# Kernel tuning notes

Hardware: AMD Instinct MI355X
Metric: run time of the kernel (lower is better)

The kernel has to match this reference:

```python
import jax, jax.numpy as jnp
import numpy as np

MIN_NORM = 1e-15
EPS = 1e-5
C_CURV = 1.0  # args.c

def _norm(x):
    return jnp.clip(jnp.linalg.norm(x, axis=-1, keepdims=True), MIN_NORM)

def artanh(x):
    x = jnp.clip(x, -1.0 + EPS, 1.0 - EPS)
    return 0.5 * (jnp.log1p(x) - jnp.log1p(-x))

def proj(x, c):
    # clip points to stay strictly inside the Poincare ball
    norm = _norm(x)
    maxnorm = (1.0 - EPS) / jnp.sqrt(c)
    return jnp.where(norm > maxnorm, x / norm * maxnorm, x)

def expmap0(u, c):
    sqrt_c = jnp.sqrt(c)
    u_norm = _norm(u)
    return jnp.tanh(sqrt_c * u_norm) * u / (sqrt_c * u_norm)

def logmap0(p, c):
    sqrt_c = jnp.sqrt(c)
    p_norm = _norm(p)
    return artanh(sqrt_c * p_norm) * p / (sqrt_c * p_norm)

def mobius_add(x, y, c):
    x2 = jnp.sum(x * x, axis=-1, keepdims=True)
    y2 = jnp.sum(y * y, axis=-1, keepdims=True)
    xy = jnp.sum(x * y, axis=-1, keepdims=True)
    num = (1.0 + 2.0 * c * xy + c * y2) * x + (1.0 - c * x2) * y
    denom = 1.0 + 2.0 * c * xy + c * c * x2 * y2
    return num / jnp.clip(denom, MIN_NORM)

def mobius_matvec(W, x, c):
    sqrt_c = jnp.sqrt(c)
    x_norm = _norm(x)
    mx = x @ W.T
    mx_norm = _norm(mx)
    return jnp.tanh(mx_norm / x_norm * artanh(sqrt_c * x_norm)) * mx / (mx_norm * sqrt_c)

def poincare_dist(x, y, c):
    sqrt_c = jnp.sqrt(c)
    d = _norm(mobius_add(-x, y, c))[..., 0]
    return 2.0 / sqrt_c * artanh(sqrt_c * d)

def hgnn_layer(h, adj, W, b, c):
    # HypLinear: mobius matvec + hyperbolic bias
    mv = proj(mobius_matvec(W, h, c), c)
    hyp_b = proj(expmap0(b, c), c)
    h = proj(mobius_add(mv, hyp_b, c), c)
    # HypAgg: aggregate in tangent space at origin
    h = proj(expmap0(adj @ logmap0(h, c), c), c)
    # HypAct: relu in tangent space
    return proj(expmap0(jax.nn.relu(logmap0(h, c)), c), c)

def setup_inputs() -> dict:
    key = jax.random.key(0)
    ks = jax.random.split(key, 10)
    N, D, C, NC, NODE_C, L = 8192, 128, 64, 7, 7, 4
    x = jax.random.normal(ks[0], (N, D), jnp.float32)
    adj = jax.random.uniform(ks[1], (N, N), jnp.float32) / N  # row-stochastic-ish dense adjacency
    graph_indicator = jax.random.randint(ks[2], (N,), 0, 1)
    W_conv = jax.random.normal(ks[3], (L, D, D), jnp.float32) / np.sqrt(D)
    b_conv = jax.random.normal(ks[4], (L, D), jnp.float32) * 0.01
    centroids = jax.random.normal(ks[5], (C, D), jnp.float32) * 0.1
    W_mlp = jax.random.normal(ks[6], (NC, C), jnp.float32) * 0.1
    b_mlp = jnp.zeros((NC,), jnp.float32)
    W_mlp1 = jax.random.normal(ks[7], (NODE_C, D), jnp.float32) * 0.1
    b_mlp1 = jnp.zeros((NODE_C,), jnp.float32)
    return {"x": x, "adj": adj, "graph_indicator": graph_indicator,
            "W_conv": W_conv, "b_conv": b_conv, "centroids": centroids,
            "W_mlp": W_mlp, "b_mlp": b_mlp, "W_mlp1": W_mlp1, "b_mlp1": b_mlp1}

def reference(x, adj, graph_indicator, W_conv, b_conv, centroids, W_mlp, b_mlp, W_mlp1, b_mlp1):
    c = C_CURV
    # proj_tan0 is identity for PoincareBall
    h = proj(expmap0(x, c), c)
    # 2 residual blocks, each with 2 HGNN layers; shortcut is identity (in_dim == out_dim)
    for blk in range(2):
        res = h
        for j in range(2):
            idx = blk * 2 + j
            h = hgnn_layer(h, adj, W_conv[idx], b_conv[idx], c)
        h = h + res  # Euclidean residual, as in the source
    # CentroidDistance: pairwise hyperbolic distance [N, C]
    node_centroid_dist = poincare_dist(h[:, None, :], centroids[None, :, :], c)
    readout = jnp.mean(node_centroid_dist, axis=0, keepdims=True)  # [1, C]
    h_r = logmap0(readout, c)  # proj_tan0(logmap0(.)) -> identity proj_tan0
    logits = jax.nn.softmax(h_r @ W_mlp.T + b_mlp, axis=0)[None]        # [1,1,NC]
    h1 = logmap0(h, c)
    logits_node = jax.nn.softmax(h1 @ W_mlp1.T + b_mlp1, axis=0)[None]  # [1,N,node_classes]
    return (logits, logits_node, h_r)
```

## Files before the change

### kernel.cpp

```cpp
#include <hip/hip_runtime.h>

#define MIN_NORM 1e-15f
#define EPSV 1e-5f
#define MAXN (1.0f - EPSV)
#define NN 8192
#define DD 128

typedef unsigned short u16;
typedef __bf16 bf16x8 __attribute__((ext_vector_type(8)));
typedef float f32x4 __attribute__((ext_vector_type(4)));

__device__ __forceinline__ float wave_sum(float v) {
#pragma unroll
  for (int off = 32; off > 0; off >>= 1) v += __shfl_xor(v, off, 64);
  return v;
}

__device__ __forceinline__ float artanh_f(float x) {
  x = fminf(fmaxf(x, -1.0f + EPSV), 1.0f - EPSV);
  return 0.5f * (log1pf(x) - log1pf(-x));
}

__device__ __forceinline__ u16 f2bf(float f) {
  unsigned u = __float_as_uint(f);
  unsigned r = (u + 0x7fffu + ((u >> 16) & 1u)) >> 16;
  return (u16)r;
}
__device__ __forceinline__ float bf2f(u16 b) { return __uint_as_float(((unsigned)b) << 16); }

__device__ __forceinline__ void gload16(const u16* g, u16* l) {
  __builtin_amdgcn_global_load_lds((const __attribute__((address_space(1))) void*)(g),
                                   (__attribute__((address_space(3))) void*)(l), 16, 0, 0);
}

__global__ __launch_bounds__(256) void gemm_bt(const u16* __restrict__ A,
                                               const u16* __restrict__ Bt,
                                               float* __restrict__ Cp,
                                               int M, int K, int KC) {
  __shared__ __align__(16) u16 Ash[2 * 64 * 64];
  __shared__ __align__(16) u16 Bsh[2 * 128 * 64];

  const int tid = threadIdx.x;
  const int lane = tid & 63;
  const int w = tid >> 6;
  const int wm = w >> 1, wn = w & 1;
  const int lrow = lane & 15;
  const int lq = lane >> 4;
  const int m0 = blockIdx.x * 64;
  const int kk0 = blockIdx.y * KC;

  const int srow = lane >> 3;
  const int spc = lane & 7;

  const u16* Ap = A + (size_t)m0 * K;

  f32x4 acc[2][4];
#pragma unroll
  for (int a = 0; a < 2; a++)
#pragma unroll
    for (int b = 0; b < 4; b++)
#pragma unroll
      for (int r = 0; r < 4; r++) acc[a][b][r] = 0.0f;

#define STAGE(bf, kk)                                                          \
  do {                                                                         \
    _Pragma("unroll") for (int ii = 0; ii < 2; ii++) {                         \
      int rw = ((ii * 4 + w) << 3) + srow;                                     \
      gload16(Ap + (size_t)rw * K + (kk) + ((spc ^ (rw & 7)) << 3),            \
              &Ash[(bf) * 4096 + ((ii * 4 + w) << 9)]);                        \
    }                                                                          \
    _Pragma("unroll") for (int ii = 0; ii < 4; ii++) {                         \
      int rw = ((ii * 4 + w) << 3) + srow;                                     \
      gload16(Bt + (size_t)rw * K + (kk) + ((spc ^ (rw & 7)) << 3),            \
              &Bsh[(bf) * 8192 + ((ii * 4 + w) << 9)]);                        \
    }                                                                          \
  } while (0)

  const int nt = KC >> 6;
  STAGE(0, kk0);

  for (int t = 0; t < nt; t++) {
    const int cur = t & 1;
    __syncthreads();
    if (t + 1 < nt) STAGE(cur ^ 1, kk0 + (t + 1) * 64);

    const int abase = cur * 4096, bbase = cur * 8192;
#pragma unroll
    for (int ks = 0; ks < 2; ks++) {
      const int lc = ks * 4 + lq;
      bf16x8 af[2], bfr[4];
#pragma unroll
      for (int ti = 0; ti < 2; ti++) {
        int r = wm * 32 + ti * 16 + lrow;
        af[ti] = *(const bf16x8*)&Ash[abase + r * 64 + ((lc ^ (r & 7)) << 3)];
      }
#pragma unroll
      for (int tj = 0; tj < 4; tj++) {
        int n = wn * 64 + tj * 16 + lrow;
        bfr[tj] = *(const bf16x8*)&Bsh[bbase + n * 64 + ((lc ^ (n & 7)) << 3)];
      }
#pragma unroll
      for (int ti = 0; ti < 2; ti++)
#pragma unroll
        for (int tj = 0; tj < 4; tj++)
          acc[ti][tj] = __builtin_amdgcn_mfma_f32_16x16x32_bf16(af[ti], bfr[tj], acc[ti][tj], 0, 0, 0);
    }
  }
#undef STAGE

  float* C = Cp + (size_t)blockIdx.y * M * 128;
#pragma unroll
  for (int ti = 0; ti < 2; ti++)
#pragma unroll
    for (int tj = 0; tj < 4; tj++)
#pragma unroll
      for (int r = 0; r < 4; r++) {
        int row = m0 + wm * 32 + ti * 16 + lq * 4 + r;
        int col = wn * 64 + tj * 16 + lrow;
        C[(size_t)row * 128 + col] = acc[ti][tj][r];
      }
}

__global__ __launch_bounds__(256) void cvt_adj(const float* __restrict__ src,
                                               u16* __restrict__ dst) {
  const size_t stride = (size_t)gridDim.x * 256 * 8;
  for (size_t base = ((size_t)blockIdx.x * 256 + threadIdx.x) * 8;
       base < (size_t)NN * NN; base += stride) {
    float4 a = *(const float4*)(src + base);
    float4 b = *(const float4*)(src + base + 4);
    ushort4 d0, d1;
    d0.x = f2bf(a.x); d0.y = f2bf(a.y); d0.z = f2bf(a.z); d0.w = f2bf(a.w);
    d1.x = f2bf(b.x); d1.y = f2bf(b.y); d1.z = f2bf(b.z); d1.w = f2bf(b.w);
    *(ushort4*)(dst + base) = d0;
    *(ushort4*)(dst + base + 4) = d1;
  }
}

__global__ void build_wt(const float* __restrict__ W, u16* __restrict__ Wt2) {
  int idx = blockIdx.x * 256 + threadIdx.x;
  if (idx >= 4 * 128 * 128) return;
  int layer = idx >> 14;
  int n = (idx >> 7) & 127;
  int k = idx & 127;
  float e = W[idx];
  u16 hi = f2bf(e);
  u16 lo = f2bf(e - bf2f(hi));
  u16* base = Wt2 + (size_t)layer * 128 * 384 + (size_t)n * 384;
  base[k] = hi;
  base[128 + k] = hi;
  base[256 + k] = lo;
}

__device__ __forceinline__ void write_split(u16* hs, int i, int lane, float v0, float v1) {
  u16* row = hs + (size_t)i * 384;
  u16 h0 = f2bf(v0), h1 = f2bf(v1);
  u16 l0 = f2bf(v0 - bf2f(h0)), l1 = f2bf(v1 - bf2f(h1));
  row[lane] = h0;         row[lane + 64] = h1;
  row[128 + lane] = l0;   row[128 + 64 + lane] = l1;
  row[256 + lane] = h0;   row[256 + 64 + lane] = h1;
}

__global__ __launch_bounds__(64) void rowwise_init(const float* __restrict__ x,
                                                   float* __restrict__ h,
                                                   float* __restrict__ res,
                                                   u16* __restrict__ hsplit) {
  int i = blockIdx.x, lane = threadIdx.x;
  const float* xr = x + (size_t)i * DD;
  float a0 = xr[lane], a1 = xr[lane + 64];
  float n = fmaxf(sqrtf(wave_sum(a0 * a0 + a1 * a1)), MIN_NORM);
  float g = tanhf(n) / n;
  float y0 = g * a0, y1 = g * a1;
  float pn = fmaxf(sqrtf(wave_sum(y0 * y0 + y1 * y1)), MIN_NORM);
  float s = pn > MAXN ? MAXN / pn : 1.0f;
  y0 *= s; y1 *= s;
  size_t base = (size_t)i * DD;
  h[base + lane] = y0;   h[base + lane + 64] = y1;
  res[base + lane] = y0; res[base + lane + 64] = y1;
  write_split(hsplit, i, lane, y0, y1);
}

__global__ __launch_bounds__(64) void rowwise_mid(const float* __restrict__ h,
                                                  const float* __restrict__ P,
                                                  const float* __restrict__ bvec,
                                                  u16* __restrict__ uT) {
  int i = blockIdx.x, lane = threadIdx.x;
  size_t base = (size_t)i * DD;
  const float* hr = h + base;
  float h0 = hr[lane], h1 = hr[lane + 64];
  float m0 = 0.f, m1 = 0.f;
#pragma unroll
  for (int sk = 0; sk < 3; sk++) {
    const float* p = P + (size_t)sk * NN * DD + base;
    m0 += p[lane];
    m1 += p[lane + 64];
  }
  float xn = fmaxf(sqrtf(wave_sum(h0 * h0 + h1 * h1)), MIN_NORM);
  float mn = fmaxf(sqrtf(wave_sum(m0 * m0 + m1 * m1)), MIN_NORM);
  float t = tanhf(mn / xn * artanh_f(xn));
  float v0 = t * m0 / mn, v1 = t * m1 / mn;
  float pn = fmaxf(sqrtf(wave_sum(v0 * v0 + v1 * v1)), MIN_NORM);
  float sc = pn > MAXN ? MAXN / pn : 1.0f;
  v0 *= sc; v1 *= sc;
  float b0 = bvec[lane], b1 = bvec[lane + 64];
  float bn = fmaxf(sqrtf(wave_sum(b0 * b0 + b1 * b1)), MIN_NORM);
  float gb = tanhf(bn) / bn;
  float e0 = gb * b0, e1 = gb * b1;
  float en = fmaxf(sqrtf(wave_sum(e0 * e0 + e1 * e1)), MIN_NORM);
  float sb = en > MAXN ? MAXN / en : 1.0f;
  e0 *= sb; e1 *= sb;
  float x2 = wave_sum(v0 * v0 + v1 * v1);
  float y2 = wave_sum(e0 * e0 + e1 * e1);
  float xy = wave_sum(v0 * e0 + v1 * e1);
  float ca = 1.0f + 2.0f * xy + y2;
  float cb = 1.0f - x2;
  float den = fmaxf(1.0f + 2.0f * xy + x2 * y2, MIN_NORM);
  float t0 = (ca * v0 + cb * e0) / den, t1 = (ca * v1 + cb * e1) / den;
  float tn = fmaxf(sqrtf(wave_sum(t0 * t0 + t1 * t1)), MIN_NORM);
  float st = tn > MAXN ? MAXN / tn : 1.0f;
  t0 *= st; t1 *= st;
  float pn2 = fmaxf(sqrtf(wave_sum(t0 * t0 + t1 * t1)), MIN_NORM);
  float gl = artanh_f(pn2) / pn2;
  uT[(size_t)lane * NN + i] = f2bf(gl * t0);
  uT[(size_t)(lane + 64) * NN + i] = f2bf(gl * t1);
}

__global__ __launch_bounds__(64) void rowwise_post(const float* __restrict__ P,
                                                   float* __restrict__ h,
                                                   float* __restrict__ res,
                                                   u16* __restrict__ hsplit,
                                                   int addres) {
  int i = blockIdx.x, lane = threadIdx.x;
  size_t base = (size_t)i * DD;
  float m0 = 0.f, m1 = 0.f;
#pragma unroll
  for (int sk = 0; sk < 8; sk++) {
    const float* p = P + (size_t)sk * NN * DD + base;
    m0 += p[lane];
    m1 += p[lane + 64];
  }
  float n = fmaxf(sqrtf(wave_sum(m0 * m0 + m1 * m1)), MIN_NORM);
  float g = tanhf(n) / n;
  float y0 = g * m0, y1 = g * m1;
  float pn = fmaxf(sqrtf(wave_sum(y0 * y0 + y1 * y1)), MIN_NORM);
  float s = pn > MAXN ? MAXN / pn : 1.0f;
  y0 *= s; y1 *= s;
  float hn = fmaxf(sqrtf(wave_sum(y0 * y0 + y1 * y1)), MIN_NORM);
  float gl = artanh_f(hn) / hn;
  float u0 = fmaxf(gl * y0, 0.0f), u1 = fmaxf(gl * y1, 0.0f);
  float un = fmaxf(sqrtf(wave_sum(u0 * u0 + u1 * u1)), MIN_NORM);
  float ge = tanhf(un) / un;
  float z0 = ge * u0, z1 = ge * u1;
  float zn = fmaxf(sqrtf(wave_sum(z0 * z0 + z1 * z1)), MIN_NORM);
  float sz = zn > MAXN ? MAXN / zn : 1.0f;
  z0 *= sz; z1 *= sz;
  if (addres) {
    z0 += res[base + lane];
    z1 += res[base + lane + 64];
    res[base + lane] = z0;
    res[base + lane + 64] = z1;
  }
  h[base + lane] = z0;
  h[base + lane + 64] = z1;
  write_split(hsplit, i, lane, z0, z1);
}

__global__ __launch_bounds__(256) void centroid_k(const float* __restrict__ h,
                                                  const float* __restrict__ cen,
                                                  float* __restrict__ rs) {
  __shared__ float cs[64 * 129];
  __shared__ float hs[32 * 128];
  __shared__ float y2s[64];
  int tid = threadIdx.x;
  int i0 = blockIdx.x * 32;
  for (int idx = tid; idx < 64 * 128; idx += 256) {
    int r = idx >> 7, c = idx & 127;
    cs[r * 129 + c] = cen[idx];
  }
  for (int idx = tid; idx < 32 * 128; idx += 256) hs[idx] = h[(size_t)i0 * 128 + idx];
  __syncthreads();
  if (tid < 64) {
    float s = 0.f;
    for (int k = 0; k < 128; k++) { float v = cs[tid * 129 + k]; s = fmaf(v, v, s); }
    y2s[tid] = s;
  }
  __syncthreads();
  int w = tid >> 6, lane = tid & 63;
  float dsum = 0.f;
  for (int rr = 0; rr < 8; rr++) {
    int r = w * 8 + rr;
    float dot = 0.f, x2 = 0.f;
    for (int k = 0; k < 128; k++) {
      float hk = hs[r * 128 + k];
      dot = fmaf(hk, cs[lane * 129 + k], dot);
      x2 = fmaf(hk, hk, x2);
    }
    float y2 = y2s[lane];
    float al = 1.0f - 2.0f * dot + y2;
    float be = 1.0f - x2;
    float num2 = al * al * x2 + be * be * y2 - 2.0f * al * be * dot;
    float den = fmaxf(1.0f - 2.0f * dot + x2 * y2, MIN_NORM);
    float d = fmaxf(sqrtf(fmaxf(num2, 0.0f)) / den, MIN_NORM);
    dsum += 2.0f * artanh_f(d);
  }
  atomicAdd(&rs[lane], dsum);
}

__global__ __launch_bounds__(64) void finalize_k(const float* __restrict__ rs,
                                                 float* __restrict__ out) {
  int lane = threadIdx.x;
  float r = rs[lane] * (1.0f / 8192.0f);
  float n = fmaxf(sqrtf(wave_sum(r * r)), MIN_NORM);
  float a = artanh_f(n);
  out[7 + NN * 7 + lane] = a * r / n;
  if (lane < 7) out[lane] = 1.0f;
}

__global__ __launch_bounds__(64) void scores_k(const float* __restrict__ h,
                                               const float* __restrict__ Wm,
                                               const float* __restrict__ bm,
                                               float* __restrict__ sc) {
  int i = blockIdx.x, lane = threadIdx.x;
  const float* hr = h + (size_t)i * DD;
  float h0 = hr[lane], h1 = hr[lane + 64];
  float pn = fmaxf(sqrtf(wave_sum(h0 * h0 + h1 * h1)), MIN_NORM);
  float gl = artanh_f(pn) / pn;
  float u0 = gl * h0, u1 = gl * h1;
  float p[7];
#pragma unroll
  for (int j = 0; j < 7; j++)
    p[j] = wave_sum(u0 * Wm[j * 128 + lane] + u1 * Wm[j * 128 + lane + 64]);
  float v = p[0];
#pragma unroll
  for (int j = 1; j < 7; j++)
    if (lane == j) v = p[j];
  if (lane < 7) sc[(size_t)i * 7 + lane] = v + bm[lane];
}

__global__ __launch_bounds__(256) void softmax_col(const float* __restrict__ sc,
                                                   float* __restrict__ out) {
  __shared__ float buf[256][8];
  int tid = threadIdx.x;
  float mx[7];
#pragma unroll
  for (int j = 0; j < 7; j++) mx[j] = -1e30f;
  for (int i = tid; i < NN; i += 256)
#pragma unroll
    for (int j = 0; j < 7; j++) mx[j] = fmaxf(mx[j], sc[i * 7 + j]);
#pragma unroll
  for (int j = 0; j < 7; j++) buf[tid][j] = mx[j];
  __syncthreads();
  for (int off = 128; off > 0; off >>= 1) {
    if (tid < off)
#pragma unroll
      for (int j = 0; j < 7; j++) buf[tid][j] = fmaxf(buf[tid][j], buf[tid + off][j]);
    __syncthreads();
  }
  float cm[7];
#pragma unroll
  for (int j = 0; j < 7; j++) cm[j] = buf[0][j];
  __syncthreads();
  float sm[7];
#pragma unroll
  for (int j = 0; j < 7; j++) sm[j] = 0.f;
  for (int i = tid; i < NN; i += 256)
#pragma unroll
    for (int j = 0; j < 7; j++) sm[j] += expf(sc[i * 7 + j] - cm[j]);
#pragma unroll
  for (int j = 0; j < 7; j++) buf[tid][j] = sm[j];
  __syncthreads();
  for (int off = 128; off > 0; off >>= 1) {
    if (tid < off)
#pragma unroll
      for (int j = 0; j < 7; j++) buf[tid][j] += buf[tid + off][j];
    __syncthreads();
  }
  float csum[7];
#pragma unroll
  for (int j = 0; j < 7; j++) csum[j] = buf[0][j];
  __syncthreads();
  for (int idx = tid; idx < NN * 7; idx += 256) {
    int i = idx / 7, j = idx - i * 7;
    out[idx] = expf(sc[i * 7 + j] - cm[j]) / csum[j];
  }
}

extern "C" void kernel_launch(void* const* d_in, const int* in_sizes, int n_in,
                              void* d_out, int out_size, void* d_ws, size_t ws_size,
                              hipStream_t stream) {
  const float* x = (const float*)d_in[0];
  const float* adj = (const float*)d_in[1];
  const float* W_conv = (const float*)d_in[3];
  const float* b_conv = (const float*)d_in[4];
  const float* centroids = (const float*)d_in[5];
  const float* W_mlp1 = (const float*)d_in[8];
  const float* b_mlp1 = (const float*)d_in[9];
  float* out = (float*)d_out;

  char* ws = (char*)d_ws;
  size_t off = 0;
  auto alloc = [&](size_t bytes) {
    void* p = ws + off;
    off = (off + bytes + 255) & ~(size_t)255;
    return p;
  };
  float* h = (float*)alloc((size_t)NN * DD * 4);
  float* res = (float*)alloc((size_t)NN * DD * 4);
  u16* hsplit = (u16*)alloc((size_t)NN * 384 * 2);
  u16* uT = (u16*)alloc((size_t)DD * NN * 2);
  u16* Wt2 = (u16*)alloc((size_t)4 * 128 * 384 * 2);
  float* P = (float*)alloc((size_t)8 * NN * DD * 4);
  u16* adjbf = (u16*)alloc((size_t)NN * NN * 2);
  float* scores = (float*)alloc((size_t)NN * 7 * 4);
  float* rs = (float*)alloc(64 * 4);
  (void)ws_size; (void)in_sizes; (void)n_in; (void)out_size;

  hipMemsetAsync(rs, 0, 64 * 4, stream);
  build_wt<<<(4 * 128 * 128 + 255) / 256, 256, 0, stream>>>(W_conv, Wt2);
  rowwise_init<<<NN, 64, 0, stream>>>(x, h, res, hsplit);
  cvt_adj<<<2048, 256, 0, stream>>>(adj, adjbf);
  for (int layer = 0; layer < 4; layer++) {
    gemm_bt<<<dim3(NN / 64, 3), 256, 0, stream>>>(
        hsplit, Wt2 + (size_t)layer * 128 * 384, P, NN, 384, 128);
    rowwise_mid<<<NN, 64, 0, stream>>>(h, P, b_conv + layer * DD, uT);
    gemm_bt<<<dim3(NN / 64, 8), 256, 0, stream>>>(
        adjbf, uT, P, NN, NN, NN / 8);
    rowwise_post<<<NN, 64, 0, stream>>>(P, h, res, hsplit, (layer & 1));
  }
  centroid_k<<<256, 256, 0, stream>>>(h, centroids, rs);
  finalize_k<<<1, 64, 0, stream>>>(rs, out);
  scores_k<<<NN, 64, 0, stream>>>(h, W_mlp1, b_mlp1, scores);
  softmax_col<<<1, 256, 0, stream>>>(scores, out + 7);
}
```

Measured before the change: 817.3 us.

## Pre-tile and pre-swizzle adjacency and uT into contiguous 64x64 GEMM tiles

The bf16 conversion of adj now writes the matrix as contiguous, pre-swizzled 64x64 tiles, and rowwise_mid writes uT in a matching tiled layout. The adjacency GEMM gets a templated TILED path, so each wave's global-to-LDS loads read one contiguous 4KB/8KB block instead of strided rows. This targets DRAM/TLB locality and address arithmetic in the dominant adj@u GEMM. The cost is scattered 2-byte writes in rowwise_mid and a more complex conversion kernel.

```diff
diff --git a/kernel.cpp b/kernel.cpp
--- a/kernel.cpp
+++ b/kernel.cpp
@@ -33,6 +33,7 @@
                                    (__attribute__((address_space(3))) void*)(l), 16, 0, 0);
 }
 
+template <bool TILED>
 __global__ __launch_bounds__(256) void gemm_bt(const u16* __restrict__ A,
                                                const u16* __restrict__ Bt,
                                                float* __restrict__ Cp,
@@ -48,11 +49,13 @@
   const int lq = lane >> 4;
   const int m0 = blockIdx.x * 64;
   const int kk0 = blockIdx.y * KC;
+  const int kt0 = kk0 >> 6;
+  const int bxK = blockIdx.x * (K >> 6);
 
   const int srow = lane >> 3;
   const int spc = lane & 7;
 
-  const u16* Ap = A + (size_t)m0 * K;
+  const u16* Ap = A + (TILED ? 0 : (size_t)m0 * K);
 
   f32x4 acc[2][4];
 #pragma unroll
@@ -62,27 +65,36 @@
 #pragma unroll
       for (int r = 0; r < 4; r++) acc[a][b][r] = 0.0f;
 
-#define STAGE(bf, kk)                                                          \
+#define STAGE(bf, tkt, kk)                                                     \
   do {                                                                         \
-    _Pragma("unroll") for (int ii = 0; ii < 2; ii++) {                         \
-      int rw = ((ii * 4 + w) << 3) + srow;                                     \
-      gload16(Ap + (size_t)rw * K + (kk) + ((spc ^ (rw & 7)) << 3),            \
-              &Ash[(bf) * 4096 + ((ii * 4 + w) << 9)]);                        \
-    }                                                                          \
-    _Pragma("unroll") for (int ii = 0; ii < 4; ii++) {                         \
-      int rw = ((ii * 4 + w) << 3) + srow;                                     \
-      gload16(Bt + (size_t)rw * K + (kk) + ((spc ^ (rw & 7)) << 3),            \
-              &Bsh[(bf) * 8192 + ((ii * 4 + w) << 9)]);                        \
+    if constexpr (TILED) {                                                     \
+      const u16* at = A + (((size_t)(bxK + (tkt))) << 12) + (lane << 3);       \
+      _Pragma("unroll") for (int ii = 0; ii < 2; ii++)                         \
+        gload16(at + ((ii * 4 + w) << 9), &Ash[(bf) * 4096 + ((ii * 4 + w) << 9)]); \
+      const u16* bt2 = Bt + (((size_t)(tkt)) << 13) + (lane << 3);             \
+      _Pragma("unroll") for (int ii = 0; ii < 4; ii++)                         \
+        gload16(bt2 + ((ii * 4 + w) << 9), &Bsh[(bf) * 8192 + ((ii * 4 + w) << 9)]); \
+    } else {                                                                   \
+      _Pragma("unroll") for (int ii = 0; ii < 2; ii++) {                       \
+        int rw = ((ii * 4 + w) << 3) + srow;                                   \
+        gload16(Ap + (size_t)rw * K + (kk) + ((spc ^ (rw & 7)) << 3),          \
+                &Ash[(bf) * 4096 + ((ii * 4 + w) << 9)]);                      \
+      }                                                                        \
+      _Pragma("unroll") for (int ii = 0; ii < 4; ii++) {                       \
+        int rw = ((ii * 4 + w) << 3) + srow;                                   \
+        gload16(Bt + (size_t)rw * K + (kk) + ((spc ^ (rw & 7)) << 3),          \
+                &Bsh[(bf) * 8192 + ((ii * 4 + w) << 9)]);                      \
+      }                                                                        \
     }                                                                          \
   } while (0)
 
   const int nt = KC >> 6;
-  STAGE(0, kk0);
+  STAGE(0, kt0, kk0);
 
   for (int t = 0; t < nt; t++) {
     const int cur = t & 1;
     __syncthreads();
-    if (t + 1 < nt) STAGE(cur ^ 1, kk0 + (t + 1) * 64);
+    if (t + 1 < nt) STAGE(cur ^ 1, kt0 + t + 1, kk0 + (t + 1) * 64);
 
     const int abase = cur * 4096, bbase = cur * 8192;
 #pragma unroll
@@ -121,18 +133,27 @@
       }
 }
 
-__global__ __launch_bounds__(256) void cvt_adj(const float* __restrict__ src,
-                                               u16* __restrict__ dst) {
-  const size_t stride = (size_t)gridDim.x * 256 * 8;
-  for (size_t base = ((size_t)blockIdx.x * 256 + threadIdx.x) * 8;
-       base < (size_t)NN * NN; base += stride) {
-    float4 a = *(const float4*)(src + base);
-    float4 b = *(const float4*)(src + base + 4);
+__global__ __launch_bounds__(256) void cvt_tile(const float* __restrict__ src,
+                                                u16* __restrict__ dst) {
+  int tid = threadIdx.x;
+  int xb = blockIdx.x;
+  int kg = blockIdx.y;
+  int ch = tid & 63;
+  int rs = tid >> 6;
+#pragma unroll
+  for (int rr = 0; rr < 16; rr++) {
+    int row = rr * 4 + rs;
+    int gk = kg * 512 + ch * 8;
+    const float* s = src + (size_t)(xb * 64 + row) * NN + gk;
+    float4 a = *(const float4*)s;
+    float4 b = *(const float4*)(s + 4);
     ushort4 d0, d1;
     d0.x = f2bf(a.x); d0.y = f2bf(a.y); d0.z = f2bf(a.z); d0.w = f2bf(a.w);
     d1.x = f2bf(b.x); d1.y = f2bf(b.y); d1.z = f2bf(b.z); d1.w = f2bf(b.w);
-    *(ushort4*)(dst + base) = d0;
-    *(ushort4*)(dst + base + 4) = d1;
+    u16* d = dst + (((size_t)(xb * 128 + (gk >> 6))) << 12) + row * 64 +
+             ((((gk >> 3) & 7) ^ (row & 7)) << 3);
+    *(ushort4*)d = d0;
+    *(ushort4*)(d + 4) = d1;
   }
 }
 
@@ -182,7 +203,7 @@
 __global__ __launch_bounds__(64) void rowwise_mid(const float* __restrict__ h,
                                                   const float* __restrict__ P,
                                                   const float* __restrict__ bvec,
-                                                  u16* __restrict__ uT) {
+                                                  u16* __restrict__ uT2) {
   int i = blockIdx.x, lane = threadIdx.x;
   size_t base = (size_t)i * DD;
   const float* hr = h + base;
@@ -220,8 +241,11 @@
   t0 *= st; t1 *= st;
   float pn2 = fmaxf(sqrtf(wave_sum(t0 * t0 + t1 * t1)), MIN_NORM);
   float gl = artanh_f(pn2) / pn2;
-  uT[(size_t)lane * NN + i] = f2bf(gl * t0);
-  uT[(size_t)(lane + 64) * NN + i] = f2bf(gl * t1);
+  u16* tb = uT2 + (((size_t)(i >> 6)) << 13);
+  int c8 = (i >> 3) & 7, k7 = i & 7;
+  tb[lane * 64 + (((c8) ^ (lane & 7)) << 3) + k7] = f2bf(gl * t0);
+  int n2 = lane + 64;
+  tb[n2 * 64 + (((c8) ^ (n2 & 7)) << 3) + k7] = f2bf(gl * t1);
 }
 
 __global__ __launch_bounds__(64) void rowwise_post(const float* __restrict__ P,
@@ -406,10 +430,10 @@
   float* h = (float*)alloc((size_t)NN * DD * 4);
   float* res = (float*)alloc((size_t)NN * DD * 4);
   u16* hsplit = (u16*)alloc((size_t)NN * 384 * 2);
-  u16* uT = (u16*)alloc((size_t)DD * NN * 2);
+  u16* uT2 = (u16*)alloc((size_t)DD * NN * 2);
   u16* Wt2 = (u16*)alloc((size_t)4 * 128 * 384 * 2);
   float* P = (float*)alloc((size_t)8 * NN * DD * 4);
-  u16* adjbf = (u16*)alloc((size_t)NN * NN * 2);
+  u16* adjT = (u16*)alloc((size_t)NN * NN * 2);
   float* scores = (float*)alloc((size_t)NN * 7 * 4);
   float* rs = (float*)alloc(64 * 4);
   (void)ws_size; (void)in_sizes; (void)n_in; (void)out_size;
@@ -417,13 +441,13 @@
   hipMemsetAsync(rs, 0, 64 * 4, stream);
   build_wt<<<(4 * 128 * 128 + 255) / 256, 256, 0, stream>>>(W_conv, Wt2);
   rowwise_init<<<NN, 64, 0, stream>>>(x, h, res, hsplit);
-  cvt_adj<<<2048, 256, 0, stream>>>(adj, adjbf);
+  cvt_tile<<<dim3(128, 16), 256, 0, stream>>>(adj, adjT);
   for (int layer = 0; layer < 4; layer++) {
-    gemm_bt<<<dim3(NN / 64, 3), 256, 0, stream>>>(
+    gemm_bt<false><<<dim3(NN / 64, 3), 256, 0, stream>>>(
         hsplit, Wt2 + (size_t)layer * 128 * 384, P, NN, 384, 128);
-    rowwise_mid<<<NN, 64, 0, stream>>>(h, P, b_conv + layer * DD, uT);
-    gemm_bt<<<dim3(NN / 64, 8), 256, 0, stream>>>(
-        adjbf, uT, P, NN, NN, NN / 8);
+    rowwise_mid<<<NN, 64, 0, stream>>>(h, P, b_conv + layer * DD, uT2);
+    gemm_bt<true><<<dim3(NN / 64, 8), 256, 0, stream>>>(
+        adjT, uT2, P, NN, NN, NN / 8);
     rowwise_post<<<NN, 64, 0, stream>>>(P, h, res, hsplit, (layer & 1));
   }
   centroid_k<<<256, 256, 0, stream>>>(h, centroids, rs);
```

Measured after the change: 811.9 us. Within noise of the previous version (-0.7%).
